# Kernel tuning notes

Hardware: AMD Instinct MI355X
Metric: run time of the kernel (lower is better)

The kernel has to match this reference:

```python
import jax, jax.numpy as jnp
import numpy as np
from jax.ops import segment_sum

N_NODES = 100000


def _gcn_layer(x, W, b, src, dst, n_nodes):
    # DGL GraphConv with norm='both': out = D_in^{-1/2} A D_out^{-1/2} x W + b
    # degrees clamped to min 1 (DGL behavior, handles zero-degree nodes)
    ones_e = jnp.ones(src.shape[0], dtype=x.dtype)
    deg_out = jnp.clip(segment_sum(ones_e, src, num_segments=n_nodes), 1.0)
    deg_in = jnp.clip(segment_sum(ones_e, dst, num_segments=n_nodes), 1.0)
    h = x * jax.lax.rsqrt(deg_out)[:, None]            # [N, F] source norm
    agg = segment_sum(h[src], dst, num_segments=n_nodes)  # [N, F] sum over in-edges
    agg = agg * jax.lax.rsqrt(deg_in)[:, None]          # dest norm
    return agg @ W + b


def setup_inputs() -> dict:
    key = jax.random.key(0)
    k1, k2, k3, k4, k5 = jax.random.split(key, 5)
    E = 1600000
    x = jax.random.normal(k1, (N_NODES, 128), dtype=jnp.float32)
    edge_src = jax.random.randint(k2, (E,), 0, N_NODES, dtype=jnp.int32)
    edge_dst = jax.random.randint(k3, (E,), 0, N_NODES, dtype=jnp.int32)
    W1 = jax.random.normal(k4, (128, 64), dtype=jnp.float32) * (1.0 / np.sqrt(128))
    b1 = jnp.zeros((64,), dtype=jnp.float32)
    W2 = jax.random.normal(k5, (64, 64), dtype=jnp.float32) * (1.0 / np.sqrt(64))
    b2 = jnp.zeros((64,), dtype=jnp.float32)
    return {"x": x, "edge_src": edge_src, "edge_dst": edge_dst,
            "W1": W1, "b1": b1, "W2": W2, "b2": b2}


def reference(x, edge_src, edge_dst, W1, b1, W2, b2):
    h = _gcn_layer(x, W1, b1, edge_src, edge_dst, N_NODES)
    h = jax.nn.relu(h)
    out = _gcn_layer(h, W2, b2, edge_src, edge_dst, N_NODES)
    return out
```

## Files before the change

### kernel.cpp

```cpp
#include <hip/hip_runtime.h>
#include <hip/hip_fp16.h>


static inline size_t align256(size_t x) { return (x + 255) & ~(size_t)255; }

#define BKT_SHIFT 8
#define BKT_W 256
#define MAX_NBK 400
#define CAP 5120
#define SC_BLOCKS 256
#define SC_THREADS 512

typedef _Float16 f16x8 __attribute__((ext_vector_type(8)));
typedef float f32x4 __attribute__((ext_vector_type(4)));

__global__ __launch_bounds__(SC_THREADS)
void scatter_atomic_kernel(const int* __restrict__ src, const int* __restrict__ dst,
                           int* __restrict__ gcnt_d, int* __restrict__ gcnt_s,
                           int* __restrict__ ebuf, unsigned char* __restrict__ sbuf,
                           int nbk, int E, int slice_len) {
    __shared__ int hd[MAX_NBK];
    __shared__ int hs[MAX_NBK];
    __shared__ int cur_d[MAX_NBK];
    __shared__ int cur_s[MAX_NBK];
    const int b = blockIdx.x;
    const int t = threadIdx.x;
    for (int i = t; i < nbk; i += SC_THREADS) { hd[i] = 0; hs[i] = 0; }
    __syncthreads();
    const int beg = b * slice_len;
    const int end = min(beg + slice_len, E);
    for (int i = beg + t; i < end; i += SC_THREADS) {
        atomicAdd(&hd[dst[i] >> BKT_SHIFT], 1);
        atomicAdd(&hs[src[i] >> BKT_SHIFT], 1);
    }
    __syncthreads();
    for (int i = t; i < nbk; i += SC_THREADS) {
        int c = hd[i];
        cur_d[i] = i * CAP + (c ? atomicAdd(&gcnt_d[i], c) : 0);
        c = hs[i];
        cur_s[i] = i * CAP + (c ? atomicAdd(&gcnt_s[i], c) : 0);
    }
    __syncthreads();
    for (int i = beg + t; i < end; i += SC_THREADS) {
        int d = dst[i], s = src[i];
        int pd = atomicAdd(&cur_d[d >> BKT_SHIFT], 1);
        ebuf[pd] = ((d & (BKT_W - 1)) << 17) | s;
        int ps = atomicAdd(&cur_s[s >> BKT_SHIFT], 1);
        sbuf[ps] = (unsigned char)(s & (BKT_W - 1));
    }
}

__global__ __launch_bounds__(512)
void bucket_csr_kernel(const int* __restrict__ ebuf,
                       const unsigned char* __restrict__ sbuf,
                       const int* __restrict__ gcnt_d, const int* __restrict__ gcnt_s,
                       int* __restrict__ csr_src,
                       int* __restrict__ cnt_in, int* __restrict__ cnt_out,
                       int* __restrict__ row_ptr,
                       int nbk, int N, int E) {
    __shared__ int cnt[BKT_W];
    __shared__ int rp[BKT_W];
    __shared__ int cur[BKT_W];
    __shared__ int cnts[BKT_W];
    __shared__ int red[512];
    __shared__ int sh_db;
    const int k = blockIdx.x;
    const int lo = k << BKT_SHIFT;
    const int span = min(BKT_W, N - lo);
    const int t = threadIdx.x;

    int s1 = 0;
    for (int i = t; i < k; i += 512) s1 += gcnt_d[i];
    red[t] = s1;
    __syncthreads();
    for (int off = 256; off >= 1; off >>= 1) {
        if (t < off) red[t] += red[t + off];
        __syncthreads();
    }
    if (t == 0) sh_db = red[0];
    __syncthreads();
    const int db = sh_db;
    const int eb = k * CAP, ee = eb + gcnt_d[k];
    const int sb = k * CAP, se = sb + gcnt_s[k];

    if (t < BKT_W) { cnt[t] = 0; cnts[t] = 0; }
    __syncthreads();
    for (int i = eb + t; i < ee; i += 512) atomicAdd(&cnt[ebuf[i] >> 17], 1);
    for (int i = sb + t; i < se; i += 512) atomicAdd(&cnts[sbuf[i]], 1);
    __syncthreads();
    if (t < BKT_W) rp[t] = cnt[t];
    __syncthreads();
    for (int off = 1; off < BKT_W; off <<= 1) {
        int v = (t < BKT_W && t >= off) ? rp[t - off] : 0;
        __syncthreads();
        if (t < BKT_W) rp[t] += v;
        __syncthreads();
    }
    if (t < span) {
        row_ptr[lo + t] = db + rp[t] - cnt[t];
        cnt_in[lo + t]  = cnt[t];
        cnt_out[lo + t] = cnts[t];
    }
    __syncthreads();
    if (t < BKT_W) cur[t] = db + rp[t] - cnt[t];
    __syncthreads();
    for (int i = eb + t; i < ee; i += 512) {
        int p = ebuf[i];
        int pos = atomicAdd(&cur[p >> 17], 1);
        csr_src[pos] = p & 0x1FFFF;
    }
    if (k == 0 && t == 0) row_ptr[N] = E;
}

template <int K>
__global__ __launch_bounds__(256)
void gemm_scale_kernel(const float* __restrict__ X, const float* __restrict__ W,
                       const int* __restrict__ cnt_out,
                       __half* __restrict__ Y, int N) {
    __shared__ _Float16 Wt[2][64][K + 8];
    const int t = threadIdx.x;
    {
        const int jj = t >> 2;
        const int kb = (t & 3) * (K / 4);
#pragma unroll
        for (int c8 = 0; c8 < K / 4; c8 += 8) {
            float w[8];
#pragma unroll
            for (int m = 0; m < 8; ++m) w[m] = W[(kb + c8 + m) * 64 + jj];
            f16x8 hi8, lo8;
#pragma unroll
            for (int m = 0; m < 8; ++m) {
                const _Float16 h = (_Float16)w[m];
                hi8[m] = h;
                lo8[m] = (_Float16)(w[m] - (float)h);
            }
            *(f16x8*)&Wt[0][jj][kb + c8] = hi8;
            *(f16x8*)&Wt[1][jj][kb + c8] = lo8;
        }
    }
    __syncthreads();

    const int wid  = t >> 6;
    const int lane = t & 63;
    const int col  = lane & 15;
    const int kg   = (lane >> 4) * 8;

    const int rowA = blockIdx.x * 64 + wid * 16 + col;
    const size_t xbase = (size_t)min(rowA, N - 1) * K;

    f32x4 acc0 = {}, acc1 = {}, acc2 = {}, acc3 = {};

#pragma unroll
    for (int ks = 0; ks < K; ks += 32) {
        float4 xa = *(const float4*)&X[xbase + ks + kg];
        float4 xb = *(const float4*)&X[xbase + ks + kg + 4];
        const float xs[8] = {xa.x, xa.y, xa.z, xa.w, xb.x, xb.y, xb.z, xb.w};
        f16x8 ahi, alo;
#pragma unroll
        for (int j = 0; j < 8; ++j) {
            const _Float16 h = (_Float16)xs[j];
            ahi[j] = h;
            alo[j] = (_Float16)(xs[j] - (float)h);
        }
#pragma unroll
        for (int tile = 0; tile < 4; ++tile) {
            const f16x8 bhi = *(const f16x8*)&Wt[0][col + 16 * tile][ks + kg];
            const f16x8 blo = *(const f16x8*)&Wt[1][col + 16 * tile][ks + kg];
            f32x4* acc = (tile == 0) ? &acc0 : (tile == 1) ? &acc1
                       : (tile == 2) ? &acc2 : &acc3;
            *acc = __builtin_amdgcn_mfma_f32_16x16x32_f16(ahi, bhi, *acc, 0, 0, 0);
            *acc = __builtin_amdgcn_mfma_f32_16x16x32_f16(alo, bhi, *acc, 0, 0, 0);
            *acc = __builtin_amdgcn_mfma_f32_16x16x32_f16(ahi, blo, *acc, 0, 0, 0);
        }
    }

    const int rbase = blockIdx.x * 64 + wid * 16 + (lane >> 4) * 4;
#pragma unroll
    for (int r = 0; r < 4; ++r) {
        const int rr = rbase + r;
        if (rr < N) {
            const float sc = rsqrtf((float)max(cnt_out[rr], 1));
            __half* yp = &Y[(size_t)rr * 64 + col];
            yp[0]  = __float2half_rn(acc0[r] * sc);
            yp[16] = __float2half_rn(acc1[r] * sc);
            yp[32] = __float2half_rn(acc2[r] * sc);
            yp[48] = __float2half_rn(acc3[r] * sc);
        }
    }
}

__global__ __launch_bounds__(256)
void agg_gemm_kernel(const __half* __restrict__ Y,
                     const int* __restrict__ row_ptr,
                     const int* __restrict__ csr_src,
                     const int* __restrict__ cnt_in,
                     const int* __restrict__ cnt_out,
                     const float* __restrict__ b1,
                     const float* __restrict__ W2,
                     __half* __restrict__ Y2, int N) {
    __shared__ _Float16 Hh[32][72];
    __shared__ _Float16 Hl[32][72];
    const int t = threadIdx.x;
    const int wid  = t >> 6;
    const int lane = t & 63;
    const int col  = lane & 15;
    const int kg   = (lane >> 4) * 8;

    const int nl = t >> 3;
    const int f8 = t & 7;
    const int n  = blockIdx.x * 32 + nl;
    const int nc = min(n, N - 1);

    const int start = row_ptr[nc];
    const int end   = row_ptr[nc + 1];
    const int last  = end - 1;

    float4 acc0 = {0.f, 0.f, 0.f, 0.f}, acc1 = {0.f, 0.f, 0.f, 0.f};
    for (int e = start; e < end; e += 8) {
        int idx[8];
#pragma unroll
        for (int j = 0; j < 8; ++j) idx[j] = csr_src[min(e + j, last)];
        uint4 v[8];
#pragma unroll
        for (int j = 0; j < 8; ++j)
            v[j] = *((const uint4*)(Y + ((size_t)idx[j] << 6)) + f8);
#pragma unroll
        for (int j = 0; j < 8; ++j) {
            if (e + j < end) {
                float2 a = __half22float2(*(const __half2*)&v[j].x);
                float2 b = __half22float2(*(const __half2*)&v[j].y);
                float2 c = __half22float2(*(const __half2*)&v[j].z);
                float2 d = __half22float2(*(const __half2*)&v[j].w);
                acc0.x += a.x; acc0.y += a.y; acc0.z += b.x; acc0.w += b.y;
                acc1.x += c.x; acc1.y += c.y; acc1.z += d.x; acc1.w += d.y;
            }
        }
    }

    float wb[16];
#pragma unroll
    for (int m = 0; m < 8; ++m) {
        wb[m]     = W2[(kg + m) * 64 + 16 * wid + col];
        wb[m + 8] = W2[(32 + kg + m) * 64 + 16 * wid + col];
    }

    {
        const float sc = rsqrtf((float)max(cnt_in[nc], 1));
        const float4 bb0 = *(const float4*)&b1[8 * f8];
        const float4 bb1 = *(const float4*)&b1[8 * f8 + 4];
        float hv[8];
        hv[0] = fmaxf(acc0.x * sc + bb0.x, 0.f);
        hv[1] = fmaxf(acc0.y * sc + bb0.y, 0.f);
        hv[2] = fmaxf(acc0.z * sc + bb0.z, 0.f);
        hv[3] = fmaxf(acc0.w * sc + bb0.w, 0.f);
        hv[4] = fmaxf(acc1.x * sc + bb1.x, 0.f);
        hv[5] = fmaxf(acc1.y * sc + bb1.y, 0.f);
        hv[6] = fmaxf(acc1.z * sc + bb1.z, 0.f);
        hv[7] = fmaxf(acc1.w * sc + bb1.w, 0.f);
        f16x8 hh, hl;
#pragma unroll
        for (int q = 0; q < 8; ++q) {
            const _Float16 hi = (_Float16)hv[q];
            hh[q] = hi;
            hl[q] = (_Float16)(hv[q] - (float)hi);
        }
        *(f16x8*)&Hh[nl][8 * f8] = hh;
        *(f16x8*)&Hl[nl][8 * f8] = hl;
    }
    __syncthreads();

    f16x8 bhi0, blo0, bhi1, blo1;
#pragma unroll
    for (int m = 0; m < 8; ++m) {
        _Float16 h = (_Float16)wb[m];
        bhi0[m] = h;
        blo0[m] = (_Float16)(wb[m] - (float)h);
        h = (_Float16)wb[m + 8];
        bhi1[m] = h;
        blo1[m] = (_Float16)(wb[m + 8] - (float)h);
    }

    const int rloc = (lane >> 4) * 4;
#pragma unroll
    for (int g = 0; g < 2; ++g) {
        const f16x8 ahi0 = *(const f16x8*)&Hh[g * 16 + col][kg];
        const f16x8 alo0 = *(const f16x8*)&Hl[g * 16 + col][kg];
        const f16x8 ahi1 = *(const f16x8*)&Hh[g * 16 + col][32 + kg];
        const f16x8 alo1 = *(const f16x8*)&Hl[g * 16 + col][32 + kg];

        f32x4 acc2 = {};
        acc2 = __builtin_amdgcn_mfma_f32_16x16x32_f16(ahi0, bhi0, acc2, 0, 0, 0);
        acc2 = __builtin_amdgcn_mfma_f32_16x16x32_f16(alo0, bhi0, acc2, 0, 0, 0);
        acc2 = __builtin_amdgcn_mfma_f32_16x16x32_f16(ahi0, blo0, acc2, 0, 0, 0);
        acc2 = __builtin_amdgcn_mfma_f32_16x16x32_f16(ahi1, bhi1, acc2, 0, 0, 0);
        acc2 = __builtin_amdgcn_mfma_f32_16x16x32_f16(alo1, bhi1, acc2, 0, 0, 0);
        acc2 = __builtin_amdgcn_mfma_f32_16x16x32_f16(ahi1, blo1, acc2, 0, 0, 0);

#pragma unroll
        for (int r = 0; r < 4; ++r) {
            const int rr = blockIdx.x * 32 + g * 16 + rloc + r;
            if (rr < N) {
                const float s2 = rsqrtf((float)max(cnt_out[rr], 1));
                Y2[(size_t)rr * 64 + 16 * wid + col] = __float2half_rn(acc2[r] * s2);
            }
        }
    }
}

template <bool RELU>
__global__ __launch_bounds__(256)
void aggregate_kernel(const __half* __restrict__ Y,
                      const int* __restrict__ row_ptr,
                      const int* __restrict__ csr_src,
                      const int* __restrict__ cnt_in,
                      const float* __restrict__ bias,
                      float* __restrict__ out, int N) {
    const int n = blockIdx.x * 32 + (threadIdx.x >> 3);
    if (n >= N) return;
    const int f8 = threadIdx.x & 7;

    const int start = row_ptr[n];
    const int end   = row_ptr[n + 1];
    const int last  = end - 1;

    float4 acc0 = {0.f, 0.f, 0.f, 0.f}, acc1 = {0.f, 0.f, 0.f, 0.f};
    for (int e = start; e < end; e += 8) {
        int idx[8];
#pragma unroll
        for (int j = 0; j < 8; ++j) idx[j] = csr_src[min(e + j, last)];
        uint4 v[8];
#pragma unroll
        for (int j = 0; j < 8; ++j)
            v[j] = *((const uint4*)(Y + ((size_t)idx[j] << 6)) + f8);
#pragma unroll
        for (int j = 0; j < 8; ++j) {
            if (e + j < end) {
                float2 a = __half22float2(*(const __half2*)&v[j].x);
                float2 b = __half22float2(*(const __half2*)&v[j].y);
                float2 c = __half22float2(*(const __half2*)&v[j].z);
                float2 d = __half22float2(*(const __half2*)&v[j].w);
                acc0.x += a.x; acc0.y += a.y; acc0.z += b.x; acc0.w += b.y;
                acc1.x += c.x; acc1.y += c.y; acc1.z += d.x; acc1.w += d.y;
            }
        }
    }

    const float sc = rsqrtf((float)max(cnt_in[n], 1));
    const float4 bb0 = *(const float4*)&bias[8 * f8];
    const float4 bb1 = *(const float4*)&bias[8 * f8 + 4];
    float4 o0, o1;
    o0.x = acc0.x * sc + bb0.x;
    o0.y = acc0.y * sc + bb0.y;
    o0.z = acc0.z * sc + bb0.z;
    o0.w = acc0.w * sc + bb0.w;
    o1.x = acc1.x * sc + bb1.x;
    o1.y = acc1.y * sc + bb1.y;
    o1.z = acc1.z * sc + bb1.z;
    o1.w = acc1.w * sc + bb1.w;
    if (RELU) {
        o0.x = fmaxf(o0.x, 0.f); o0.y = fmaxf(o0.y, 0.f);
        o0.z = fmaxf(o0.z, 0.f); o0.w = fmaxf(o0.w, 0.f);
        o1.x = fmaxf(o1.x, 0.f); o1.y = fmaxf(o1.y, 0.f);
        o1.z = fmaxf(o1.z, 0.f); o1.w = fmaxf(o1.w, 0.f);
    }
    float4* op = (float4*)&out[((size_t)n << 6) + 8 * f8];
    op[0] = o0;
    op[1] = o1;
}

extern "C" void kernel_launch(void* const* d_in, const int* in_sizes, int n_in,
                              void* d_out, int out_size, void* d_ws, size_t ws_size,
                              hipStream_t stream) {
    const float* x   = (const float*)d_in[0];
    const int*   src = (const int*)d_in[1];
    const int*   dst = (const int*)d_in[2];
    const float* W1  = (const float*)d_in[3];
    const float* b1  = (const float*)d_in[4];
    const float* W2  = (const float*)d_in[5];
    const float* b2  = (const float*)d_in[6];
    float* out = (float*)d_out;

    const int N = in_sizes[0] / 128;
    const int E = in_sizes[1];

    const int nbk = (N + BKT_W - 1) >> BKT_SHIFT;

    char* ws = (char*)d_ws;
    size_t off = 0;
    __half* Y       = (__half*)(ws + off); off = align256(off + (size_t)N * 64 * sizeof(__half));
    __half* Y2      = (__half*)(ws + off); off = align256(off + (size_t)N * 64 * sizeof(__half));
    int* csr_src    = (int*)(ws + off);    off = align256(off + (size_t)E * sizeof(int));
    int* ebuf       = (int*)(ws + off);    off = align256(off + (size_t)nbk * CAP * sizeof(int));
    unsigned char* sbuf = (unsigned char*)(ws + off); off = align256(off + (size_t)nbk * CAP);
    int* gcnt       = (int*)(ws + off);    off = align256(off + (size_t)2 * nbk * sizeof(int));
    int* gcnt_d     = gcnt;
    int* gcnt_s     = gcnt + nbk;
    int* cnt_out    = (int*)(ws + off);    off = align256(off + (size_t)N * sizeof(int));
    int* cnt_in     = (int*)(ws + off);    off = align256(off + (size_t)N * sizeof(int));
    int* row_ptr    = (int*)(ws + off);    off = align256(off + (size_t)(N + 1) * sizeof(int));

    const int pslice = (E + SC_BLOCKS - 1) / SC_BLOCKS;

    hipMemsetAsync(gcnt, 0, (size_t)2 * nbk * sizeof(int), stream);
    scatter_atomic_kernel<<<SC_BLOCKS, SC_THREADS, 0, stream>>>(
        src, dst, gcnt_d, gcnt_s, ebuf, sbuf, nbk, E, pslice);
    bucket_csr_kernel<<<nbk, 512, 0, stream>>>(ebuf, sbuf, gcnt_d, gcnt_s, csr_src,
                                               cnt_in, cnt_out, row_ptr, nbk, N, E);

    const int gemm_blocks = (N + 63) / 64;
    const int agg_blocks  = (N + 31) / 32;

    gemm_scale_kernel<128><<<gemm_blocks, 256, 0, stream>>>(x, W1, cnt_out, Y, N);
    agg_gemm_kernel<<<agg_blocks, 256, 0, stream>>>(Y, row_ptr, csr_src,
                                                    cnt_in, cnt_out, b1, W2, Y2, N);
    aggregate_kernel<false><<<agg_blocks, 256, 0, stream>>>(Y2, row_ptr, csr_src,
                                                            cnt_in, b2, out, N);
}
```

Baseline: 240.6 us.

## Merge all graph stages into one cooperative persistent kernel with grid syncs

Replaces the memset plus five separate kernel launches (partition, CSR build, GEMM, aggregate+GEMM, aggregate) with one cooperative persistent kernel. The stages are separated by grid-wide syncs, and the shared memory of each stage is overlaid in a union. The aim is to remove launch gaps and the memset. The cost is a grid capped by occupancy (at most 512 blocks) that loops over work, 512-thread blocks with a tighter register budget, and grid.sync overhead. Load balance in the irregular aggregation phases may be worse than with a full oversubscribed grid.

```diff
diff --git a/kernel.cpp b/kernel.cpp
--- a/kernel.cpp
+++ b/kernel.cpp
@@ -1,5 +1,8 @@
 #include <hip/hip_runtime.h>
 #include <hip/hip_fp16.h>
+#include <hip/hip_cooperative_groups.h>
+
+namespace cg = cooperative_groups;
 
 
 static inline size_t align256(size_t x) { return (x + 255) & ~(size_t)255; }
@@ -8,364 +11,339 @@
 #define BKT_W 256
 #define MAX_NBK 400
 #define CAP 5120
-#define SC_BLOCKS 256
-#define SC_THREADS 512
+#define MG_THREADS 512
+#define MG_MAX_BLOCKS 512
 
 typedef _Float16 f16x8 __attribute__((ext_vector_type(8)));
 typedef float f32x4 __attribute__((ext_vector_type(4)));
 
-__global__ __launch_bounds__(SC_THREADS)
-void scatter_atomic_kernel(const int* __restrict__ src, const int* __restrict__ dst,
-                           int* __restrict__ gcnt_d, int* __restrict__ gcnt_s,
-                           int* __restrict__ ebuf, unsigned char* __restrict__ sbuf,
-                           int nbk, int E, int slice_len) {
-    __shared__ int hd[MAX_NBK];
-    __shared__ int hs[MAX_NBK];
-    __shared__ int cur_d[MAX_NBK];
-    __shared__ int cur_s[MAX_NBK];
+__global__ __launch_bounds__(MG_THREADS, 4)
+void mega_kernel(const float* __restrict__ x,
+                 const int* __restrict__ src, const int* __restrict__ dst,
+                 const float* __restrict__ W1, const float* __restrict__ b1,
+                 const float* __restrict__ W2, const float* __restrict__ b2,
+                 float* __restrict__ out,
+                 __half* __restrict__ Y, __half* __restrict__ Y2,
+                 int* __restrict__ csr_src, int* __restrict__ ebuf,
+                 unsigned char* __restrict__ sbuf,
+                 int* __restrict__ gcnt_d, int* __restrict__ gcnt_s,
+                 int* __restrict__ cnt_in, int* __restrict__ cnt_out,
+                 int* __restrict__ row_ptr,
+                 int N, int E, int nbk)
+{
+    cg::grid_group grid = cg::this_grid();
+    const int t = threadIdx.x;
     const int b = blockIdx.x;
-    const int t = threadIdx.x;
-    for (int i = t; i < nbk; i += SC_THREADS) { hd[i] = 0; hs[i] = 0; }
-    __syncthreads();
-    const int beg = b * slice_len;
-    const int end = min(beg + slice_len, E);
-    for (int i = beg + t; i < end; i += SC_THREADS) {
-        atomicAdd(&hd[dst[i] >> BKT_SHIFT], 1);
-        atomicAdd(&hs[src[i] >> BKT_SHIFT], 1);
-    }
-    __syncthreads();
-    for (int i = t; i < nbk; i += SC_THREADS) {
-        int c = hd[i];
-        cur_d[i] = i * CAP + (c ? atomicAdd(&gcnt_d[i], c) : 0);
-        c = hs[i];
-        cur_s[i] = i * CAP + (c ? atomicAdd(&gcnt_s[i], c) : 0);
-    }
-    __syncthreads();
-    for (int i = beg + t; i < end; i += SC_THREADS) {
-        int d = dst[i], s = src[i];
-        int pd = atomicAdd(&cur_d[d >> BKT_SHIFT], 1);
-        ebuf[pd] = ((d & (BKT_W - 1)) << 17) | s;
-        int ps = atomicAdd(&cur_s[s >> BKT_SHIFT], 1);
-        sbuf[ps] = (unsigned char)(s & (BKT_W - 1));
-    }
-}
-
-__global__ __launch_bounds__(512)
-void bucket_csr_kernel(const int* __restrict__ ebuf,
-                       const unsigned char* __restrict__ sbuf,
-                       const int* __restrict__ gcnt_d, const int* __restrict__ gcnt_s,
-                       int* __restrict__ csr_src,
-                       int* __restrict__ cnt_in, int* __restrict__ cnt_out,
-                       int* __restrict__ row_ptr,
-                       int nbk, int N, int E) {
-    __shared__ int cnt[BKT_W];
-    __shared__ int rp[BKT_W];
-    __shared__ int cur[BKT_W];
-    __shared__ int cnts[BKT_W];
-    __shared__ int red[512];
-    __shared__ int sh_db;
-    const int k = blockIdx.x;
-    const int lo = k << BKT_SHIFT;
-    const int span = min(BKT_W, N - lo);
-    const int t = threadIdx.x;
-
-    int s1 = 0;
-    for (int i = t; i < k; i += 512) s1 += gcnt_d[i];
-    red[t] = s1;
-    __syncthreads();
-    for (int off = 256; off >= 1; off >>= 1) {
-        if (t < off) red[t] += red[t + off];
-        __syncthreads();
-    }
-    if (t == 0) sh_db = red[0];
-    __syncthreads();
-    const int db = sh_db;
-    const int eb = k * CAP, ee = eb + gcnt_d[k];
-    const int sb = k * CAP, se = sb + gcnt_s[k];
-
-    if (t < BKT_W) { cnt[t] = 0; cnts[t] = 0; }
-    __syncthreads();
-    for (int i = eb + t; i < ee; i += 512) atomicAdd(&cnt[ebuf[i] >> 17], 1);
-    for (int i = sb + t; i < se; i += 512) atomicAdd(&cnts[sbuf[i]], 1);
-    __syncthreads();
-    if (t < BKT_W) rp[t] = cnt[t];
-    __syncthreads();
-    for (int off = 1; off < BKT_W; off <<= 1) {
-        int v = (t < BKT_W && t >= off) ? rp[t - off] : 0;
-        __syncthreads();
-        if (t < BKT_W) rp[t] += v;
-        __syncthreads();
-    }
-    if (t < span) {
-        row_ptr[lo + t] = db + rp[t] - cnt[t];
-        cnt_in[lo + t]  = cnt[t];
-        cnt_out[lo + t] = cnts[t];
-    }
-    __syncthreads();
-    if (t < BKT_W) cur[t] = db + rp[t] - cnt[t];
-    __syncthreads();
-    for (int i = eb + t; i < ee; i += 512) {
-        int p = ebuf[i];
-        int pos = atomicAdd(&cur[p >> 17], 1);
-        csr_src[pos] = p & 0x1FFFF;
-    }
-    if (k == 0 && t == 0) row_ptr[N] = E;
-}
-
-template <int K>
-__global__ __launch_bounds__(256)
-void gemm_scale_kernel(const float* __restrict__ X, const float* __restrict__ W,
-                       const int* __restrict__ cnt_out,
-                       __half* __restrict__ Y, int N) {
-    __shared__ _Float16 Wt[2][64][K + 8];
-    const int t = threadIdx.x;
-    {
-        const int jj = t >> 2;
-        const int kb = (t & 3) * (K / 4);
-#pragma unroll
-        for (int c8 = 0; c8 < K / 4; c8 += 8) {
-            float w[8];
-#pragma unroll
-            for (int m = 0; m < 8; ++m) w[m] = W[(kb + c8 + m) * 64 + jj];
-            f16x8 hi8, lo8;
-#pragma unroll
-            for (int m = 0; m < 8; ++m) {
-                const _Float16 h = (_Float16)w[m];
-                hi8[m] = h;
-                lo8[m] = (_Float16)(w[m] - (float)h);
-            }
-            *(f16x8*)&Wt[0][jj][kb + c8] = hi8;
-            *(f16x8*)&Wt[1][jj][kb + c8] = lo8;
-        }
-    }
-    __syncthreads();
-
-    const int wid  = t >> 6;
+    const int nblocks = gridDim.x;
+
+    __shared__ union {
+        struct { int hd[MAX_NBK], hs[MAX_NBK], cd[MAX_NBK], cs[MAX_NBK]; } part;
+        struct { int cnt[BKT_W], rp[BKT_W], cur[BKT_W], cnts[BKT_W],
+                 red[MG_THREADS], db; } csr;
+        struct { _Float16 Wt[2][64][136]; } gemm;
+        struct { _Float16 Hh[64][72], Hl[64][72]; } fuse;
+    } u;
+
     const int lane = t & 63;
     const int col  = lane & 15;
     const int kg   = (lane >> 4) * 8;
 
-    const int rowA = blockIdx.x * 64 + wid * 16 + col;
-    const size_t xbase = (size_t)min(rowA, N - 1) * K;
-
-    f32x4 acc0 = {}, acc1 = {}, acc2 = {}, acc3 = {};
-
-#pragma unroll
-    for (int ks = 0; ks < K; ks += 32) {
-        float4 xa = *(const float4*)&X[xbase + ks + kg];
-        float4 xb = *(const float4*)&X[xbase + ks + kg + 4];
-        const float xs[8] = {xa.x, xa.y, xa.z, xa.w, xb.x, xb.y, xb.z, xb.w};
-        f16x8 ahi, alo;
-#pragma unroll
-        for (int j = 0; j < 8; ++j) {
-            const _Float16 h = (_Float16)xs[j];
-            ahi[j] = h;
-            alo[j] = (_Float16)(xs[j] - (float)h);
-        }
-#pragma unroll
-        for (int tile = 0; tile < 4; ++tile) {
-            const f16x8 bhi = *(const f16x8*)&Wt[0][col + 16 * tile][ks + kg];
-            const f16x8 blo = *(const f16x8*)&Wt[1][col + 16 * tile][ks + kg];
-            f32x4* acc = (tile == 0) ? &acc0 : (tile == 1) ? &acc1
-                       : (tile == 2) ? &acc2 : &acc3;
-            *acc = __builtin_amdgcn_mfma_f32_16x16x32_f16(ahi, bhi, *acc, 0, 0, 0);
-            *acc = __builtin_amdgcn_mfma_f32_16x16x32_f16(alo, bhi, *acc, 0, 0, 0);
-            *acc = __builtin_amdgcn_mfma_f32_16x16x32_f16(ahi, blo, *acc, 0, 0, 0);
-        }
-    }
-
-    const int rbase = blockIdx.x * 64 + wid * 16 + (lane >> 4) * 4;
-#pragma unroll
-    for (int r = 0; r < 4; ++r) {
-        const int rr = rbase + r;
-        if (rr < N) {
-            const float sc = rsqrtf((float)max(cnt_out[rr], 1));
-            __half* yp = &Y[(size_t)rr * 64 + col];
-            yp[0]  = __float2half_rn(acc0[r] * sc);
-            yp[16] = __float2half_rn(acc1[r] * sc);
-            yp[32] = __float2half_rn(acc2[r] * sc);
-            yp[48] = __float2half_rn(acc3[r] * sc);
-        }
-    }
-}
-
-__global__ __launch_bounds__(256)
-void agg_gemm_kernel(const __half* __restrict__ Y,
-                     const int* __restrict__ row_ptr,
-                     const int* __restrict__ csr_src,
-                     const int* __restrict__ cnt_in,
-                     const int* __restrict__ cnt_out,
-                     const float* __restrict__ b1,
-                     const float* __restrict__ W2,
-                     __half* __restrict__ Y2, int N) {
-    __shared__ _Float16 Hh[32][72];
-    __shared__ _Float16 Hl[32][72];
-    const int t = threadIdx.x;
-    const int wid  = t >> 6;
-    const int lane = t & 63;
-    const int col  = lane & 15;
-    const int kg   = (lane >> 4) * 8;
-
-    const int nl = t >> 3;
-    const int f8 = t & 7;
-    const int n  = blockIdx.x * 32 + nl;
-    const int nc = min(n, N - 1);
-
-    const int start = row_ptr[nc];
-    const int end   = row_ptr[nc + 1];
-    const int last  = end - 1;
-
-    float4 acc0 = {0.f, 0.f, 0.f, 0.f}, acc1 = {0.f, 0.f, 0.f, 0.f};
-    for (int e = start; e < end; e += 8) {
-        int idx[8];
-#pragma unroll
-        for (int j = 0; j < 8; ++j) idx[j] = csr_src[min(e + j, last)];
-        uint4 v[8];
-#pragma unroll
-        for (int j = 0; j < 8; ++j)
-            v[j] = *((const uint4*)(Y + ((size_t)idx[j] << 6)) + f8);
-#pragma unroll
-        for (int j = 0; j < 8; ++j) {
-            if (e + j < end) {
-                float2 a = __half22float2(*(const __half2*)&v[j].x);
-                float2 b = __half22float2(*(const __half2*)&v[j].y);
-                float2 c = __half22float2(*(const __half2*)&v[j].z);
-                float2 d = __half22float2(*(const __half2*)&v[j].w);
-                acc0.x += a.x; acc0.y += a.y; acc0.z += b.x; acc0.w += b.y;
-                acc1.x += c.x; acc1.y += c.y; acc1.z += d.x; acc1.w += d.y;
-            }
-        }
-    }
-
-    float wb[16];
-#pragma unroll
-    for (int m = 0; m < 8; ++m) {
-        wb[m]     = W2[(kg + m) * 64 + 16 * wid + col];
-        wb[m + 8] = W2[(32 + kg + m) * 64 + 16 * wid + col];
-    }
-
     {
-        const float sc = rsqrtf((float)max(cnt_in[nc], 1));
-        const float4 bb0 = *(const float4*)&b1[8 * f8];
-        const float4 bb1 = *(const float4*)&b1[8 * f8 + 4];
-        float hv[8];
-        hv[0] = fmaxf(acc0.x * sc + bb0.x, 0.f);
-        hv[1] = fmaxf(acc0.y * sc + bb0.y, 0.f);
-        hv[2] = fmaxf(acc0.z * sc + bb0.z, 0.f);
-        hv[3] = fmaxf(acc0.w * sc + bb0.w, 0.f);
-        hv[4] = fmaxf(acc1.x * sc + bb1.x, 0.f);
-        hv[5] = fmaxf(acc1.y * sc + bb1.y, 0.f);
-        hv[6] = fmaxf(acc1.z * sc + bb1.z, 0.f);
-        hv[7] = fmaxf(acc1.w * sc + bb1.w, 0.f);
-        f16x8 hh, hl;
-#pragma unroll
-        for (int q = 0; q < 8; ++q) {
-            const _Float16 hi = (_Float16)hv[q];
-            hh[q] = hi;
-            hl[q] = (_Float16)(hv[q] - (float)hi);
-        }
-        *(f16x8*)&Hh[nl][8 * f8] = hh;
-        *(f16x8*)&Hl[nl][8 * f8] = hl;
-    }
-    __syncthreads();
-
-    f16x8 bhi0, blo0, bhi1, blo1;
-#pragma unroll
-    for (int m = 0; m < 8; ++m) {
-        _Float16 h = (_Float16)wb[m];
-        bhi0[m] = h;
-        blo0[m] = (_Float16)(wb[m] - (float)h);
-        h = (_Float16)wb[m + 8];
-        bhi1[m] = h;
-        blo1[m] = (_Float16)(wb[m + 8] - (float)h);
-    }
-
-    const int rloc = (lane >> 4) * 4;
-#pragma unroll
-    for (int g = 0; g < 2; ++g) {
-        const f16x8 ahi0 = *(const f16x8*)&Hh[g * 16 + col][kg];
-        const f16x8 alo0 = *(const f16x8*)&Hl[g * 16 + col][kg];
-        const f16x8 ahi1 = *(const f16x8*)&Hh[g * 16 + col][32 + kg];
-        const f16x8 alo1 = *(const f16x8*)&Hl[g * 16 + col][32 + kg];
-
-        f32x4 acc2 = {};
-        acc2 = __builtin_amdgcn_mfma_f32_16x16x32_f16(ahi0, bhi0, acc2, 0, 0, 0);
-        acc2 = __builtin_amdgcn_mfma_f32_16x16x32_f16(alo0, bhi0, acc2, 0, 0, 0);
-        acc2 = __builtin_amdgcn_mfma_f32_16x16x32_f16(ahi0, blo0, acc2, 0, 0, 0);
-        acc2 = __builtin_amdgcn_mfma_f32_16x16x32_f16(ahi1, bhi1, acc2, 0, 0, 0);
-        acc2 = __builtin_amdgcn_mfma_f32_16x16x32_f16(alo1, bhi1, acc2, 0, 0, 0);
-        acc2 = __builtin_amdgcn_mfma_f32_16x16x32_f16(ahi1, blo1, acc2, 0, 0, 0);
-
-#pragma unroll
-        for (int r = 0; r < 4; ++r) {
-            const int rr = blockIdx.x * 32 + g * 16 + rloc + r;
-            if (rr < N) {
-                const float s2 = rsqrtf((float)max(cnt_out[rr], 1));
-                Y2[(size_t)rr * 64 + 16 * wid + col] = __float2half_rn(acc2[r] * s2);
-            }
-        }
-    }
-}
-
-template <bool RELU>
-__global__ __launch_bounds__(256)
-void aggregate_kernel(const __half* __restrict__ Y,
-                      const int* __restrict__ row_ptr,
-                      const int* __restrict__ csr_src,
-                      const int* __restrict__ cnt_in,
-                      const float* __restrict__ bias,
-                      float* __restrict__ out, int N) {
-    const int n = blockIdx.x * 32 + (threadIdx.x >> 3);
-    if (n >= N) return;
-    const int f8 = threadIdx.x & 7;
-
-    const int start = row_ptr[n];
-    const int end   = row_ptr[n + 1];
-    const int last  = end - 1;
-
-    float4 acc0 = {0.f, 0.f, 0.f, 0.f}, acc1 = {0.f, 0.f, 0.f, 0.f};
-    for (int e = start; e < end; e += 8) {
-        int idx[8];
-#pragma unroll
-        for (int j = 0; j < 8; ++j) idx[j] = csr_src[min(e + j, last)];
-        uint4 v[8];
-#pragma unroll
-        for (int j = 0; j < 8; ++j)
-            v[j] = *((const uint4*)(Y + ((size_t)idx[j] << 6)) + f8);
-#pragma unroll
-        for (int j = 0; j < 8; ++j) {
-            if (e + j < end) {
-                float2 a = __half22float2(*(const __half2*)&v[j].x);
-                float2 b = __half22float2(*(const __half2*)&v[j].y);
-                float2 c = __half22float2(*(const __half2*)&v[j].z);
-                float2 d = __half22float2(*(const __half2*)&v[j].w);
-                acc0.x += a.x; acc0.y += a.y; acc0.z += b.x; acc0.w += b.y;
-                acc1.x += c.x; acc1.y += c.y; acc1.z += d.x; acc1.w += d.y;
-            }
-        }
-    }
-
-    const float sc = rsqrtf((float)max(cnt_in[n], 1));
-    const float4 bb0 = *(const float4*)&bias[8 * f8];
-    const float4 bb1 = *(const float4*)&bias[8 * f8 + 4];
-    float4 o0, o1;
-    o0.x = acc0.x * sc + bb0.x;
-    o0.y = acc0.y * sc + bb0.y;
-    o0.z = acc0.z * sc + bb0.z;
-    o0.w = acc0.w * sc + bb0.w;
-    o1.x = acc1.x * sc + bb1.x;
-    o1.y = acc1.y * sc + bb1.y;
-    o1.z = acc1.z * sc + bb1.z;
-    o1.w = acc1.w * sc + bb1.w;
-    if (RELU) {
-        o0.x = fmaxf(o0.x, 0.f); o0.y = fmaxf(o0.y, 0.f);
-        o0.z = fmaxf(o0.z, 0.f); o0.w = fmaxf(o0.w, 0.f);
-        o1.x = fmaxf(o1.x, 0.f); o1.y = fmaxf(o1.y, 0.f);
-        o1.z = fmaxf(o1.z, 0.f); o1.w = fmaxf(o1.w, 0.f);
-    }
-    float4* op = (float4*)&out[((size_t)n << 6) + 8 * f8];
-    op[0] = o0;
-    op[1] = o1;
+        for (int i = b * MG_THREADS + t; i < 2 * nbk; i += nblocks * MG_THREADS)
+            gcnt_d[i] = 0;
+        for (int i = t; i < nbk; i += MG_THREADS) { u.part.hd[i] = 0; u.part.hs[i] = 0; }
+        __syncthreads();
+        const int slice = (E + nblocks - 1) / nblocks;
+        const int beg = b * slice;
+        const int iend = min(beg + slice, E);
+        for (int i = beg + t; i < iend; i += MG_THREADS) {
+            atomicAdd(&u.part.hd[dst[i] >> BKT_SHIFT], 1);
+            atomicAdd(&u.part.hs[src[i] >> BKT_SHIFT], 1);
+        }
+        __syncthreads();
+        __threadfence();
+        grid.sync();
+        for (int i = t; i < nbk; i += MG_THREADS) {
+            int c = u.part.hd[i];
+            u.part.cd[i] = i * CAP + (c ? atomicAdd(&gcnt_d[i], c) : 0);
+            c = u.part.hs[i];
+            u.part.cs[i] = i * CAP + (c ? atomicAdd(&gcnt_s[i], c) : 0);
+        }
+        __syncthreads();
+        for (int i = beg + t; i < iend; i += MG_THREADS) {
+            int d = dst[i], s = src[i];
+            int pd = atomicAdd(&u.part.cd[d >> BKT_SHIFT], 1);
+            ebuf[pd] = ((d & (BKT_W - 1)) << 17) | s;
+            int ps = atomicAdd(&u.part.cs[s >> BKT_SHIFT], 1);
+            sbuf[ps] = (unsigned char)(s & (BKT_W - 1));
+        }
+    }
+    __threadfence();
+    grid.sync();
+
+    for (int k = b; k < nbk; k += nblocks) {
+        const int lo = k << BKT_SHIFT;
+        const int span = min(BKT_W, N - lo);
+        int s1 = 0;
+        for (int i = t; i < k; i += MG_THREADS) s1 += gcnt_d[i];
+        u.csr.red[t] = s1;
+        __syncthreads();
+        for (int off = MG_THREADS / 2; off >= 1; off >>= 1) {
+            if (t < off) u.csr.red[t] += u.csr.red[t + off];
+            __syncthreads();
+        }
+        if (t == 0) u.csr.db = u.csr.red[0];
+        __syncthreads();
+        const int db = u.csr.db;
+        const int eb = k * CAP, ee = eb + gcnt_d[k];
+        const int sb = k * CAP, se = sb + gcnt_s[k];
+
+        if (t < BKT_W) { u.csr.cnt[t] = 0; u.csr.cnts[t] = 0; }
+        __syncthreads();
+        for (int i = eb + t; i < ee; i += MG_THREADS) atomicAdd(&u.csr.cnt[ebuf[i] >> 17], 1);
+        for (int i = sb + t; i < se; i += MG_THREADS) atomicAdd(&u.csr.cnts[sbuf[i]], 1);
+        __syncthreads();
+        if (t < BKT_W) u.csr.rp[t] = u.csr.cnt[t];
+        __syncthreads();
+        for (int off = 1; off < BKT_W; off <<= 1) {
+            int v = (t < BKT_W && t >= off) ? u.csr.rp[t - off] : 0;
+            __syncthreads();
+            if (t < BKT_W) u.csr.rp[t] += v;
+            __syncthreads();
+        }
+        if (t < span) {
+            row_ptr[lo + t] = db + u.csr.rp[t] - u.csr.cnt[t];
+            cnt_in[lo + t]  = u.csr.cnt[t];
+            cnt_out[lo + t] = u.csr.cnts[t];
+        }
+        __syncthreads();
+        if (t < BKT_W) u.csr.cur[t] = db + u.csr.rp[t] - u.csr.cnt[t];
+        __syncthreads();
+        for (int i = eb + t; i < ee; i += MG_THREADS) {
+            int p = ebuf[i];
+            int pos = atomicAdd(&u.csr.cur[p >> 17], 1);
+            csr_src[pos] = p & 0x1FFFF;
+        }
+        if (k == 0 && t == 0) row_ptr[N] = E;
+        __syncthreads();
+    }
+    __threadfence();
+    grid.sync();
+
+    {
+        if (t < 256) {
+            const int jj = t >> 2;
+            const int kb = (t & 3) * 32;
+            for (int c8 = 0; c8 < 32; c8 += 8) {
+                float w[8];
+#pragma unroll
+                for (int m = 0; m < 8; ++m) w[m] = W1[(kb + c8 + m) * 64 + jj];
+                f16x8 hi8, lo8;
+#pragma unroll
+                for (int m = 0; m < 8; ++m) {
+                    const _Float16 h = (_Float16)w[m];
+                    hi8[m] = h;
+                    lo8[m] = (_Float16)(w[m] - (float)h);
+                }
+                *(f16x8*)&u.gemm.Wt[0][jj][kb + c8] = hi8;
+                *(f16x8*)&u.gemm.Wt[1][jj][kb + c8] = lo8;
+            }
+        }
+        __syncthreads();
+        const int w8  = t >> 6;
+        const int sub = w8 >> 2;
+        const int wid = w8 & 3;
+        for (int tb = b * 128; tb < N; tb += nblocks * 128) {
+            const int rowA = tb + sub * 64 + wid * 16 + col;
+            const size_t xbase = (size_t)min(rowA, N - 1) * 128;
+            f32x4 a0 = {}, a1 = {}, a2 = {}, a3 = {};
+#pragma unroll
+            for (int ks = 0; ks < 128; ks += 32) {
+                float4 xa = *(const float4*)&x[xbase + ks + kg];
+                float4 xb = *(const float4*)&x[xbase + ks + kg + 4];
+                const float xs[8] = {xa.x, xa.y, xa.z, xa.w, xb.x, xb.y, xb.z, xb.w};
+                f16x8 ahi, alo;
+#pragma unroll
+                for (int j = 0; j < 8; ++j) {
+                    const _Float16 h = (_Float16)xs[j];
+                    ahi[j] = h;
+                    alo[j] = (_Float16)(xs[j] - (float)h);
+                }
+#pragma unroll
+                for (int tile = 0; tile < 4; ++tile) {
+                    const f16x8 bhi = *(const f16x8*)&u.gemm.Wt[0][col + 16 * tile][ks + kg];
+                    const f16x8 blo = *(const f16x8*)&u.gemm.Wt[1][col + 16 * tile][ks + kg];
+                    f32x4* acc = (tile == 0) ? &a0 : (tile == 1) ? &a1
+                               : (tile == 2) ? &a2 : &a3;
+                    *acc = __builtin_amdgcn_mfma_f32_16x16x32_f16(ahi, bhi, *acc, 0, 0, 0);
+                    *acc = __builtin_amdgcn_mfma_f32_16x16x32_f16(alo, bhi, *acc, 0, 0, 0);
+                    *acc = __builtin_amdgcn_mfma_f32_16x16x32_f16(ahi, blo, *acc, 0, 0, 0);
+                }
+            }
+            const int rbase = tb + sub * 64 + wid * 16 + (lane >> 4) * 4;
+#pragma unroll
+            for (int r = 0; r < 4; ++r) {
+                const int rr = rbase + r;
+                if (rr < N) {
+                    const float sc = rsqrtf((float)max(cnt_out[rr], 1));
+                    __half* yp = &Y[(size_t)rr * 64 + col];
+                    yp[0]  = __float2half_rn(a0[r] * sc);
+                    yp[16] = __float2half_rn(a1[r] * sc);
+                    yp[32] = __float2half_rn(a2[r] * sc);
+                    yp[48] = __float2half_rn(a3[r] * sc);
+                }
+            }
+        }
+    }
+    __threadfence();
+    grid.sync();
+
+    {
+        const int w8 = t >> 6;
+        const int cw = w8 & 3;
+        float wb[16];
+#pragma unroll
+        for (int m = 0; m < 8; ++m) {
+            wb[m]     = W2[(kg + m) * 64 + 16 * cw + col];
+            wb[m + 8] = W2[(32 + kg + m) * 64 + 16 * cw + col];
+        }
+        f16x8 bhi0, blo0, bhi1, blo1;
+#pragma unroll
+        for (int m = 0; m < 8; ++m) {
+            _Float16 h = (_Float16)wb[m];
+            bhi0[m] = h; blo0[m] = (_Float16)(wb[m] - (float)h);
+            h = (_Float16)wb[m + 8];
+            bhi1[m] = h; blo1[m] = (_Float16)(wb[m + 8] - (float)h);
+        }
+        const int nl = t >> 3;
+        const int f8 = t & 7;
+        const int rloc = (lane >> 4) * 4;
+        for (int nb = b * 64; nb < N; nb += nblocks * 64) {
+            const int nc = min(nb + nl, N - 1);
+            const int start = row_ptr[nc];
+            const int endr  = row_ptr[nc + 1];
+            const int last  = endr - 1;
+            float4 acc0 = {0.f, 0.f, 0.f, 0.f}, acc1 = {0.f, 0.f, 0.f, 0.f};
+            for (int e = start; e < endr; e += 8) {
+                int idx[8];
+#pragma unroll
+                for (int j = 0; j < 8; ++j) idx[j] = csr_src[min(e + j, last)];
+                uint4 v[8];
+#pragma unroll
+                for (int j = 0; j < 8; ++j)
+                    v[j] = *((const uint4*)(Y + ((size_t)idx[j] << 6)) + f8);
+#pragma unroll
+                for (int j = 0; j < 8; ++j) {
+                    if (e + j < endr) {
+                        float2 aa = __half22float2(*(const __half2*)&v[j].x);
+                        float2 bb = __half22float2(*(const __half2*)&v[j].y);
+                        float2 cc = __half22float2(*(const __half2*)&v[j].z);
+                        float2 dd = __half22float2(*(const __half2*)&v[j].w);
+                        acc0.x += aa.x; acc0.y += aa.y; acc0.z += bb.x; acc0.w += bb.y;
+                        acc1.x += cc.x; acc1.y += cc.y; acc1.z += dd.x; acc1.w += dd.y;
+                    }
+                }
+            }
+            {
+                const float sc = rsqrtf((float)max(cnt_in[nc], 1));
+                const float4 bb0 = *(const float4*)&b1[8 * f8];
+                const float4 bb1 = *(const float4*)&b1[8 * f8 + 4];
+                float hv[8];
+                hv[0] = fmaxf(acc0.x * sc + bb0.x, 0.f);
+                hv[1] = fmaxf(acc0.y * sc + bb0.y, 0.f);
+                hv[2] = fmaxf(acc0.z * sc + bb0.z, 0.f);
+                hv[3] = fmaxf(acc0.w * sc + bb0.w, 0.f);
+                hv[4] = fmaxf(acc1.x * sc + bb1.x, 0.f);
+                hv[5] = fmaxf(acc1.y * sc + bb1.y, 0.f);
+                hv[6] = fmaxf(acc1.z * sc + bb1.z, 0.f);
+                hv[7] = fmaxf(acc1.w * sc + bb1.w, 0.f);
+                f16x8 hh, hl;
+#pragma unroll
+                for (int q = 0; q < 8; ++q) {
+                    const _Float16 hi = (_Float16)hv[q];
+                    hh[q] = hi;
+                    hl[q] = (_Float16)(hv[q] - (float)hi);
+                }
+                *(f16x8*)&u.fuse.Hh[nl][8 * f8] = hh;
+                *(f16x8*)&u.fuse.Hl[nl][8 * f8] = hl;
+            }
+            __syncthreads();
+#pragma unroll
+            for (int gq = 0; gq < 2; ++gq) {
+                const int g = (w8 >> 2) + 2 * gq;
+                const f16x8 ahi0 = *(const f16x8*)&u.fuse.Hh[g * 16 + col][kg];
+                const f16x8 alo0 = *(const f16x8*)&u.fuse.Hl[g * 16 + col][kg];
+                const f16x8 ahi1 = *(const f16x8*)&u.fuse.Hh[g * 16 + col][32 + kg];
+                const f16x8 alo1 = *(const f16x8*)&u.fuse.Hl[g * 16 + col][32 + kg];
+                f32x4 a2v = {};
+                a2v = __builtin_amdgcn_mfma_f32_16x16x32_f16(ahi0, bhi0, a2v, 0, 0, 0);
+                a2v = __builtin_amdgcn_mfma_f32_16x16x32_f16(alo0, bhi0, a2v, 0, 0, 0);
+                a2v = __builtin_amdgcn_mfma_f32_16x16x32_f16(ahi0, blo0, a2v, 0, 0, 0);
+                a2v = __builtin_amdgcn_mfma_f32_16x16x32_f16(ahi1, bhi1, a2v, 0, 0, 0);
+                a2v = __builtin_amdgcn_mfma_f32_16x16x32_f16(alo1, bhi1, a2v, 0, 0, 0);
+                a2v = __builtin_amdgcn_mfma_f32_16x16x32_f16(ahi1, blo1, a2v, 0, 0, 0);
+#pragma unroll
+                for (int r = 0; r < 4; ++r) {
+                    const int rr = nb + g * 16 + rloc + r;
+                    if (rr < N) {
+                        const float s2 = rsqrtf((float)max(cnt_out[rr], 1));
+                        Y2[(size_t)rr * 64 + 16 * cw + col] = __float2half_rn(a2v[r] * s2);
+                    }
+                }
+            }
+            __syncthreads();
+        }
+    }
+    __threadfence();
+    grid.sync();
+
+    {
+        const int nl = t >> 3;
+        const int f8 = t & 7;
+        for (int nb = b * 64; nb < N; nb += nblocks * 64) {
+            const int n = nb + nl;
+            if (n >= N) continue;
+            const int start = row_ptr[n];
+            const int endr  = row_ptr[n + 1];
+            const int last  = endr - 1;
+            float4 acc0 = {0.f, 0.f, 0.f, 0.f}, acc1 = {0.f, 0.f, 0.f, 0.f};
+            for (int e = start; e < endr; e += 8) {
+                int idx[8];
+#pragma unroll
+                for (int j = 0; j < 8; ++j) idx[j] = csr_src[min(e + j, last)];
+                uint4 v[8];
+#pragma unroll
+                for (int j = 0; j < 8; ++j)
+                    v[j] = *((const uint4*)(Y2 + ((size_t)idx[j] << 6)) + f8);
+#pragma unroll
+                for (int j = 0; j < 8; ++j) {
+                    if (e + j < endr) {
+                        float2 aa = __half22float2(*(const __half2*)&v[j].x);
+                        float2 bb = __half22float2(*(const __half2*)&v[j].y);
+                        float2 cc = __half22float2(*(const __half2*)&v[j].z);
+                        float2 dd = __half22float2(*(const __half2*)&v[j].w);
+                        acc0.x += aa.x; acc0.y += aa.y; acc0.z += bb.x; acc0.w += bb.y;
+                        acc1.x += cc.x; acc1.y += cc.y; acc1.z += dd.x; acc1.w += dd.y;
+                    }
+                }
+            }
+            const float sc = rsqrtf((float)max(cnt_in[n], 1));
+            const float4 bb0 = *(const float4*)&b2[8 * f8];
+            const float4 bb1 = *(const float4*)&b2[8 * f8 + 4];
+            float4 o0, o1;
+            o0.x = acc0.x * sc + bb0.x;
+            o0.y = acc0.y * sc + bb0.y;
+            o0.z = acc0.z * sc + bb0.z;
+            o0.w = acc0.w * sc + bb0.w;
+            o1.x = acc1.x * sc + bb1.x;
+            o1.y = acc1.y * sc + bb1.y;
+            o1.z = acc1.z * sc + bb1.z;
+            o1.w = acc1.w * sc + bb1.w;
+            float4* op = (float4*)&out[((size_t)n << 6) + 8 * f8];
+            op[0] = o0;
+            op[1] = o1;
+        }
+    }
 }
 
 extern "C" void kernel_launch(void* const* d_in, const int* in_sizes, int n_in,
@@ -380,10 +358,9 @@
     const float* b2  = (const float*)d_in[6];
     float* out = (float*)d_out;
 
-    const int N = in_sizes[0] / 128;
-    const int E = in_sizes[1];
-
-    const int nbk = (N + BKT_W - 1) >> BKT_SHIFT;
+    int N = in_sizes[0] / 128;
+    int E = in_sizes[1];
+    int nbk = (N + BKT_W - 1) >> BKT_SHIFT;
 
     char* ws = (char*)d_ws;
     size_t off = 0;
@@ -399,20 +376,21 @@
     int* cnt_in     = (int*)(ws + off);    off = align256(off + (size_t)N * sizeof(int));
     int* row_ptr    = (int*)(ws + off);    off = align256(off + (size_t)(N + 1) * sizeof(int));
 
-    const int pslice = (E + SC_BLOCKS - 1) / SC_BLOCKS;
-
-    hipMemsetAsync(gcnt, 0, (size_t)2 * nbk * sizeof(int), stream);
-    scatter_atomic_kernel<<<SC_BLOCKS, SC_THREADS, 0, stream>>>(
-        src, dst, gcnt_d, gcnt_s, ebuf, sbuf, nbk, E, pslice);
-    bucket_csr_kernel<<<nbk, 512, 0, stream>>>(ebuf, sbuf, gcnt_d, gcnt_s, csr_src,
-                                               cnt_in, cnt_out, row_ptr, nbk, N, E);
-
-    const int gemm_blocks = (N + 63) / 64;
-    const int agg_blocks  = (N + 31) / 32;
-
-    gemm_scale_kernel<128><<<gemm_blocks, 256, 0, stream>>>(x, W1, cnt_out, Y, N);
-    agg_gemm_kernel<<<agg_blocks, 256, 0, stream>>>(Y, row_ptr, csr_src,
-                                                    cnt_in, cnt_out, b1, W2, Y2, N);
-    aggregate_kernel<false><<<agg_blocks, 256, 0, stream>>>(Y2, row_ptr, csr_src,
-                                                            cnt_in, b2, out, N);
+    static int s_blocks = -1;
+    if (s_blocks < 0) {
+        hipDeviceProp_t prop;
+        hipGetDeviceProperties(&prop, 0);
+        int nb = 0;
+        hipOccupancyMaxActiveBlocksPerMultiprocessor(&nb, mega_kernel, MG_THREADS, 0);
+        if (nb < 1) nb = 1;
+        long cap = (long)nb * prop.multiProcessorCount;
+        s_blocks = (int)((cap < MG_MAX_BLOCKS) ? cap : MG_MAX_BLOCKS);
+    }
+
+    void* args[] = {&x, &src, &dst, &W1, &b1, &W2, &b2, &out,
+                    &Y, &Y2, &csr_src, &ebuf, &sbuf,
+                    &gcnt_d, &gcnt_s, &cnt_in, &cnt_out, &row_ptr,
+                    &N, &E, &nbk};
+    hipLaunchCooperativeKernel((const void*)mega_kernel, dim3(s_blocks),
+                               dim3(MG_THREADS), args, 0, stream);
 }
```

New measurement: 723.3 us. 201% more time.
